# Optimization experiments

Hardware: AMD Instinct MI355X
Metric: run time of the kernel (lower is better)

Reference implementation:

```python
import jax, jax.numpy as jnp
import numpy as np

H, V, B, S = 2048, 32000, 16, 256

def setup_inputs() -> dict:
    key = jax.random.key(0)
    k1, k2, k3, k4 = jax.random.split(key, 4)
    # Parameters exactly as the torch __init__ builds them
    alpha_exp = jax.nn.softmax(jax.random.normal(k1, (H, H), dtype=jnp.float32), axis=1)   # transition probs [H,H]
    beta = jax.nn.log_softmax(jax.random.normal(k2, (H, V), dtype=jnp.float32), axis=1)    # emission log-probs [H,V]
    gamma = jax.nn.log_softmax(jax.random.normal(k3, (H,), dtype=jnp.float32), axis=0)     # initial-state logits [H]
    input_ids = jax.random.randint(k4, (B, S), 0, V)
    return {"input_ids": input_ids, "alpha_exp": alpha_exp, "beta": beta, "gamma": gamma}


def _hmm_forward(input_ids, alpha_exp, beta, gamma):
    # gamma stored as log-probs; forward re-softmaxes it (faithful to torch code)
    gamma_exp = jax.nn.softmax(gamma)                       # [H]
    ids = input_ids.T                                       # [S,B]
    mask = (ids != -1).astype(beta.dtype)                   # [S,B]; -1 = padding
    # input_probs[t,h,b] = beta[h, ids[t,b]] * mask
    ip = jnp.transpose(beta[:, ids], (1, 0, 2)) * mask[:, None, :]   # [S,H,B]
    ip_rev = ip[::-1]                                       # process t = S-1 .. 0

    def step(y, ipt):
        # log-domain backward recursion: y' = log(alpha_exp @ exp(y - ymax)) + ymax + emission
        ymax = jnp.max(y, axis=0, keepdims=True)            # [1,B]
        y = jnp.log(alpha_exp @ jnp.exp(y - ymax)) + ymax + ipt
        return y, y

    y0 = ip_rev[0]                                          # t = S-1: y starts at 0, += emission
    y_last, ys_rest = jax.lax.scan(step, y0, ip_rev[1:])
    ys = jnp.concatenate([y0[None], ys_rest], axis=0)       # [S,H,B], ys[i] is t = S-1-i

    ymax = jnp.max(y_last, axis=0)                          # [B]
    final = jnp.log(gamma_exp @ jnp.exp(y_last - ymax[None, :])) + ymax   # [B] per-seq loglik
    return ys, final


def reference(input_ids, alpha_exp, beta, gamma):
    return _hmm_forward(input_ids, alpha_exp, beta, gamma)
```

## Files before the change

### kernel.cpp

```cpp
#include <hip/hip_runtime.h>
#include <cstdint>
#include <cstddef>

#define Hh 2048
#define Vv 32000
#define Bb 16
#define Ss 256

typedef unsigned short ushort_t;
typedef unsigned int   uint_t;
typedef unsigned long long ull_t;

typedef __attribute__((ext_vector_type(8))) short short8;
typedef __attribute__((ext_vector_type(4))) float f32x4;

#define Z_SLOT   ((size_t)Bb * Hh * 2)
#define WS_NEED  ((size_t)3 * Z_SLOT)

#define LD_REL(p)     __hip_atomic_load((p), __ATOMIC_RELAXED, __HIP_MEMORY_SCOPE_AGENT)
#define ST_REL(p, v)  __hip_atomic_store((p), (v), __ATOMIC_RELAXED, __HIP_MEMORY_SCOPE_AGENT)

#define SGN64 0x8000800080008000ull
#define MAG64 0x7FFF7FFF7FFF7FFFull

__device__ __forceinline__ float b2f_u(uint_t u) {
  union { uint_t u; float f; } x; x.u = u; return x.f;
}
__device__ __forceinline__ ushort_t f2b(float f) {
  union { float f; uint_t u; } x; x.f = f;
  uint_t u = x.u;
  return (ushort_t)((u + 0x7FFFu + ((u >> 16) & 1u)) >> 16);
}
__device__ __forceinline__ uint_t umaxu(uint_t a, uint_t b) { return a > b ? a : b; }
__device__ __forceinline__ uint_t pkmax16(uint_t a, uint_t b) {
  uint_t lo = umaxu(a & 0xFFFFu, b & 0xFFFFu);
  uint_t hi = umaxu(a >> 16, b >> 16);
  return lo | (hi << 16);
}

__global__ __launch_bounds__(256, 1) void hmm_persist(
    const float* __restrict__ alpha,
    const float* __restrict__ beta,
    const int*  __restrict__ ids,
    const float* __restrict__ gamma,
    ushort_t* __restrict__ Zbuf,
    float* __restrict__ out)
{
  const int w    = blockIdx.x;
  const int g    = w & 7;
  const int wl   = w >> 3;
  const int c0   = g * 2;
  const int tid  = threadIdx.x;
  const int wv   = tid >> 6;
  const int lane = tid & 63;
  const int lrow = lane & 15;
  const int quad = lane >> 4;

  __shared__ __align__(16) ushort_t zTf[2 * 2080];
  __shared__ float ybuf[128];
  __shared__ float ipld[128];
  __shared__ uint_t redm[4];
  __shared__ __align__(16) float red[4][4][256];
  __shared__ float fred[4][4];
  __shared__ float mh2[2];

  ull_t* ZbA = (ull_t*)Zbuf;

  short8 afr[64];
  #pragma unroll
  for (int t = 0; t < 4; ++t) {
    #pragma unroll
    for (int kt = 0; kt < 16; ++kt) {
      const float* arow = alpha + (size_t)(wl * 64 + t * 16 + lrow) * Hh
                          + wv * 512 + kt * 32 + quad * 8;
      float4 f0 = *(const float4*)arow;
      float4 f1 = *(const float4*)(arow + 4);
      short8 fr;
      fr[0] = (short)f2b(f0.x); fr[1] = (short)f2b(f0.y);
      fr[2] = (short)f2b(f0.z); fr[3] = (short)f2b(f0.w);
      fr[4] = (short)f2b(f1.x); fr[5] = (short)f2b(f1.y);
      fr[6] = (short)f2b(f1.z); fr[7] = (short)f2b(f1.w);
      afr[t * 16 + kt] = fr;
    }
  }

  const int myc = tid & 1;
  const int myr = wl * 64 + (tid >> 1);
  float ipreg = 0.f;

  {
    if (tid < 128) {
      const int v = ids[(c0 + myc) * Ss + (Ss - 1)];
      float yv = beta[(size_t)myr * Vv + v];
      ybuf[tid] = yv;
      out[(size_t)myr * Bb + (c0 + myc)] = yv;
    }
    __syncthreads();
    if (tid < 32) {
      const int c = tid >> 4, q = tid & 15;
      uint_t b0 = f2b(__expf(ybuf[(q * 4 + 0) * 2 + c]));
      uint_t b1 = f2b(__expf(ybuf[(q * 4 + 1) * 2 + c]));
      uint_t b2 = f2b(__expf(ybuf[(q * 4 + 2) * 2 + c]));
      uint_t b3 = f2b(__expf(ybuf[(q * 4 + 3) * 2 + c]));
      ull_t val = (ull_t)(b0 | (b1 << 16)) | ((ull_t)(b2 | (b3 << 16)) << 32);
      ST_REL(ZbA + (size_t)(c0 + c) * 512 + (wl * 16 + q), val);
    }
    if (tid < 128) {
      const int v1 = ids[(c0 + myc) * Ss + (Ss - 2)];
      ipreg = beta[(size_t)myr * Vv + v1];
    }
  }

  const size_t go0 = (size_t)c0 * 512 + tid;
  const size_t go1 = (size_t)c0 * 512 + 256 + tid;
  const size_t go2 = (size_t)(c0 + 1) * 512 + tid;
  const size_t go3 = (size_t)(c0 + 1) * 512 + 256 + tid;

  float mprev = 0.f;
  const ushort_t* zbase = zTf + (lrow & 1) * 2080 + quad * 8;

  const int  ec  = lrow;
  const int  rb  = wl * 64 + wv * 16 + quad * 4;
  const bool act = (lrow < 2);
  float pendy[4] = {0.f, 0.f, 0.f, 0.f};

  for (int k = 1; k < Ss; ++k) {
    const int   physR = (3 - ((k - 1) % 3)) % 3;
    const ull_t expS  = ((k - 1) & 1) ? SGN64 : 0ull;
    const size_t sb   = (size_t)physR * 8192;

    ull_t z0 = LD_REL(ZbA + sb + go0), z1 = LD_REL(ZbA + sb + go1);
    ull_t z2 = LD_REL(ZbA + sb + go2), z3 = LD_REL(ZbA + sb + go3);
    while ((((z0 ^ expS) | (z1 ^ expS) | (z2 ^ expS) | (z3 ^ expS)) & SGN64) != 0ull) {
      if ((z0 & SGN64) != expS) z0 = LD_REL(ZbA + sb + go0);
      if ((z1 & SGN64) != expS) z1 = LD_REL(ZbA + sb + go1);
      if ((z2 & SGN64) != expS) z2 = LD_REL(ZbA + sb + go2);
      if ((z3 & SGN64) != expS) z3 = LD_REL(ZbA + sb + go3);
    }

    uint_t m0, m1;
    {
      const ull_t u0 = z0 & MAG64, u1 = z1 & MAG64;
      const ull_t u2 = z2 & MAG64, u3 = z3 & MAG64;
      *(ull_t*)(zTf + tid * 4)               = u0;
      *(ull_t*)(zTf + 1024 + tid * 4)        = u1;
      *(ull_t*)(zTf + 2080 + tid * 4)        = u2;
      *(ull_t*)(zTf + 2080 + 1024 + tid * 4) = u3;
      uint_t t0 = pkmax16(pkmax16((uint_t)u0, (uint_t)(u0 >> 32)),
                          pkmax16((uint_t)u1, (uint_t)(u1 >> 32)));
      uint_t t1 = pkmax16(pkmax16((uint_t)u2, (uint_t)(u2 >> 32)),
                          pkmax16((uint_t)u3, (uint_t)(u3 >> 32)));
      m0 = umaxu(t0 & 0xFFFFu, t0 >> 16);
      m1 = umaxu(t1 & 0xFFFFu, t1 >> 16);
    }
    if (tid < 128) ipld[tid] = ipreg;
    uint_t pk = m0 | (m1 << 16);
    #pragma unroll
    for (int d = 1; d < 64; d <<= 1)
      pk = pkmax16(pk, (uint_t)__shfl_xor((int)pk, d));
    if (lane == 0) redm[wv] = pk;
    __syncthreads();

    if (k > 1 && act) {
      #pragma unroll
      for (int i = 0; i < 4; ++i)
        out[(size_t)(k - 1) * (Hh * Bb) + (size_t)(rb + i) * Bb + (c0 + ec)] = pendy[i];
    }

    float ipv[4];
    #pragma unroll
    for (int i = 0; i < 4; ++i)
      ipv[i] = ipld[(wv * 16 + quad * 4 + i) * 2 + (lrow & 1)];
    const uint_t rr = pkmax16(pkmax16(redm[0], redm[1]),
                              pkmax16(redm[2], redm[3]));
    const uint_t mm = (lrow & 1) ? (rr >> 16) : (rr & 0xFFFFu);
    const float lmax = __logf(b2f_u(mm << 16));

    if (k < Ss - 1 && tid < 128) {
      const int v = ids[(c0 + myc) * Ss + (Ss - 2 - k)];
      ipreg = beta[(size_t)myr * Vv + v];
    }

    f32x4 acc0 = {0.f, 0.f, 0.f, 0.f}, acc1 = acc0, acc2 = acc0, acc3 = acc0;
    #pragma unroll
    for (int kt = 0; kt < 16; ++kt) {
      short8 bfr = *(const short8*)(zbase + (wv * 16 + kt) * 32);
      acc0 = __builtin_amdgcn_mfma_f32_16x16x32_bf16(afr[kt],      bfr, acc0, 0, 0, 0);
      acc1 = __builtin_amdgcn_mfma_f32_16x16x32_bf16(afr[16 + kt], bfr, acc1, 0, 0, 0);
      acc2 = __builtin_amdgcn_mfma_f32_16x16x32_bf16(afr[32 + kt], bfr, acc2, 0, 0, 0);
      acc3 = __builtin_amdgcn_mfma_f32_16x16x32_bf16(afr[48 + kt], bfr, acc3, 0, 0, 0);
    }

    if (wv != 0) *(f32x4*)&red[0][wv][lane * 4] = acc0;
    if (wv != 1) *(f32x4*)&red[1][wv][lane * 4] = acc1;
    if (wv != 2) *(f32x4*)&red[2][wv][lane * 4] = acc2;
    if (wv != 3) *(f32x4*)&red[3][wv][lane * 4] = acc3;
    __syncthreads();
    f32x4 sf = acc0;
    if (wv == 1) sf = acc1;
    else if (wv == 2) sf = acc2;
    else if (wv == 3) sf = acc3;
    #pragma unroll
    for (int v = 0; v < 4; ++v)
      if (v != wv) sf += *(const f32x4*)&red[wv][v][lane * 4];

    const float mnew = mprev + lmax;
    if (act) {
      #pragma unroll
      for (int i = 0; i < 4; ++i)
        pendy[i] = __logf(sf[i]) + mprev + ipv[i];
      uint_t o0 = (uint_t)f2b(__expf(pendy[0] - mnew)) |
                  ((uint_t)f2b(__expf(pendy[1] - mnew)) << 16);
      uint_t o1 = (uint_t)f2b(__expf(pendy[2] - mnew)) |
                  ((uint_t)f2b(__expf(pendy[3] - mnew)) << 16);
      const int   physW = (3 - (k % 3)) % 3;
      const ull_t orS   = (k & 1) ? SGN64 : 0ull;
      ST_REL(ZbA + (size_t)physW * 8192 + (size_t)(c0 + ec) * 512 + (rb >> 2),
             ((ull_t)o0 | ((ull_t)o1 << 32)) | orS);
    }
    mprev = mnew;
  }

  if (act) {
    #pragma unroll
    for (int i = 0; i < 4; ++i)
      out[(size_t)(Ss - 1) * (Hh * Bb) + (size_t)(rb + i) * Bb + (c0 + ec)] = pendy[i];
  }

  if (wl == 0) {
    if (tid < 2) mh2[tid] = mprev;
    __syncthreads();
    float4 ga = *(const float4*)(gamma + 4 * tid);
    float4 gb = *(const float4*)(gamma + 1024 + 4 * tid);
    float gmx = fmaxf(fmaxf(fmaxf(ga.x, ga.y), fmaxf(ga.z, ga.w)),
                      fmaxf(fmaxf(gb.x, gb.y), fmaxf(gb.z, gb.w)));
    #pragma unroll
    for (int d = 1; d < 64; d <<= 1) gmx = fmaxf(gmx, __shfl_xor(gmx, d));
    if (lane == 0) fred[wv][0] = gmx;
    __syncthreads();
    const float gm = fmaxf(fmaxf(fred[0][0], fred[1][0]),
                           fmaxf(fred[2][0], fred[3][0]));
    float wgt[8];
    wgt[0] = __expf(ga.x - gm); wgt[1] = __expf(ga.y - gm);
    wgt[2] = __expf(ga.z - gm); wgt[3] = __expf(ga.w - gm);
    wgt[4] = __expf(gb.x - gm); wgt[5] = __expf(gb.y - gm);
    wgt[6] = __expf(gb.z - gm); wgt[7] = __expf(gb.w - gm);
    float s1 = ((wgt[0] + wgt[1]) + (wgt[2] + wgt[3])) +
               ((wgt[4] + wgt[5]) + (wgt[6] + wgt[7]));
    ull_t z0 = LD_REL(ZbA + go0), z1 = LD_REL(ZbA + go1);
    ull_t z2 = LD_REL(ZbA + go2), z3 = LD_REL(ZbA + go3);
    while ((((z0 ^ SGN64) | (z1 ^ SGN64) | (z2 ^ SGN64) | (z3 ^ SGN64)) & SGN64) != 0ull) {
      if ((z0 & SGN64) != SGN64) z0 = LD_REL(ZbA + go0);
      if ((z1 & SGN64) != SGN64) z1 = LD_REL(ZbA + go1);
      if ((z2 & SGN64) != SGN64) z2 = LD_REL(ZbA + go2);
      if ((z3 & SGN64) != SGN64) z3 = LD_REL(ZbA + go3);
    }
    float s2a = 0.f, s2b = 0.f;
    #pragma unroll
    for (int i = 0; i < 4; ++i) {
      s2a += wgt[i]     * b2f_u(((uint_t)(z0 >> (16 * i)) & 0x7FFFu) << 16);
      s2a += wgt[4 + i] * b2f_u(((uint_t)(z1 >> (16 * i)) & 0x7FFFu) << 16);
      s2b += wgt[i]     * b2f_u(((uint_t)(z2 >> (16 * i)) & 0x7FFFu) << 16);
      s2b += wgt[4 + i] * b2f_u(((uint_t)(z3 >> (16 * i)) & 0x7FFFu) << 16);
    }
    #pragma unroll
    for (int d = 1; d < 64; d <<= 1) {
      s1  += __shfl_xor(s1, d);
      s2a += __shfl_xor(s2a, d);
      s2b += __shfl_xor(s2b, d);
    }
    if (lane == 0) { fred[wv][1] = s1; fred[wv][2] = s2a; fred[wv][3] = s2b; }
    __syncthreads();
    if (tid == 0) {
      float S1 = ((fred[0][1] + fred[1][1]) + (fred[2][1] + fred[3][1]));
      float Sa = ((fred[0][2] + fred[1][2]) + (fred[2][2] + fred[3][2]));
      float Sb = ((fred[0][3] + fred[1][3]) + (fred[2][3] + fred[3][3]));
      const float ls1 = __logf(S1);
      out[(size_t)Ss * Hh * Bb + c0]     = __logf(Sa) - ls1 + mh2[0];
      out[(size_t)Ss * Hh * Bb + c0 + 1] = __logf(Sb) - ls1 + mh2[1];
    }
  }
}

extern "C" void kernel_launch(void* const* d_in, const int* in_sizes, int n_in,
                              void* d_out, int out_size, void* d_ws, size_t ws_size,
                              hipStream_t stream) {
  (void)in_sizes; (void)n_in; (void)out_size;
  const int*   ids   = (const int*)d_in[0];
  const float* alpha = (const float*)d_in[1];
  const float* beta  = (const float*)d_in[2];
  const float* gamma = (const float*)d_in[3];
  float* out = (float*)d_out;
  char* ws = (char*)d_ws;

  if (ws_size < WS_NEED) return;

  ushort_t* Zbuf = (ushort_t*)ws;

  hipMemsetAsync(ws, 0x80, 2 * Z_SLOT, stream);
  hipMemsetAsync(ws + 2 * Z_SLOT, 0x00, Z_SLOT, stream);

  {
    const float* a_alpha = alpha;
    const float* a_beta  = beta;
    const int*   a_ids   = ids;
    const float* a_gamma = gamma;
    ushort_t* a_z = Zbuf;  float* a_out = out;
    void* args[] = {(void*)&a_alpha, (void*)&a_beta, (void*)&a_ids,
                    (void*)&a_gamma, (void*)&a_z, (void*)&a_out};
    hipError_t e = hipLaunchCooperativeKernel((const void*)hmm_persist,
                                              dim3(256), dim3(256), args, 0, stream);
    if (e != hipSuccess) {
      hipLaunchKernelGGL(hmm_persist, dim3(256), dim3(256), 0, stream,
                         alpha, beta, ids, gamma, Zbuf, out);
    }
  }
}
```

Measured before the change: 1.761 ms.

## Remove one per-step block barrier via double-buffered LDS and wave-local Z staging

```diff
diff --git a/kernel.cpp b/kernel.cpp
--- a/kernel.cpp
+++ b/kernel.cpp
@@ -58,9 +58,9 @@
 
   __shared__ __align__(16) ushort_t zTf[2 * 2080];
   __shared__ float ybuf[128];
-  __shared__ float ipld[128];
-  __shared__ uint_t redm[4];
-  __shared__ __align__(16) float red[4][4][256];
+  __shared__ float ipld[2][128];
+  __shared__ uint_t redm[2][4];
+  __shared__ __align__(16) float red[2][4][4][256];
   __shared__ float fred[4][4];
   __shared__ float mh2[2];
 
@@ -109,12 +109,15 @@
       const int v1 = ids[(c0 + myc) * Ss + (Ss - 2)];
       ipreg = beta[(size_t)myr * Vv + v1];
     }
-  }
-
-  const size_t go0 = (size_t)c0 * 512 + tid;
-  const size_t go1 = (size_t)c0 * 512 + 256 + tid;
-  const size_t go2 = (size_t)(c0 + 1) * 512 + tid;
-  const size_t go3 = (size_t)(c0 + 1) * 512 + 256 + tid;
+    __syncthreads();
+  }
+
+  const int h4a = wv * 128 + lane;
+  const int h4b = h4a + 64;
+  const size_t go0 = (size_t)c0 * 512 + h4a;
+  const size_t go1 = (size_t)c0 * 512 + h4b;
+  const size_t go2 = (size_t)(c0 + 1) * 512 + h4a;
+  const size_t go3 = (size_t)(c0 + 1) * 512 + h4b;
 
   float mprev = 0.f;
   const ushort_t* zbase = zTf + (lrow & 1) * 2080 + quad * 8;
@@ -125,6 +128,7 @@
   float pendy[4] = {0.f, 0.f, 0.f, 0.f};
 
   for (int k = 1; k < Ss; ++k) {
+    const int   pb    = k & 1;
     const int   physR = (3 - ((k - 1) % 3)) % 3;
     const ull_t expS  = ((k - 1) & 1) ? SGN64 : 0ull;
     const size_t sb   = (size_t)physR * 8192;
@@ -142,10 +146,10 @@
     {
       const ull_t u0 = z0 & MAG64, u1 = z1 & MAG64;
       const ull_t u2 = z2 & MAG64, u3 = z3 & MAG64;
-      *(ull_t*)(zTf + tid * 4)               = u0;
-      *(ull_t*)(zTf + 1024 + tid * 4)        = u1;
-      *(ull_t*)(zTf + 2080 + tid * 4)        = u2;
-      *(ull_t*)(zTf + 2080 + 1024 + tid * 4) = u3;
+      *(ull_t*)(zTf + 4 * h4a)        = u0;
+      *(ull_t*)(zTf + 4 * h4b)        = u1;
+      *(ull_t*)(zTf + 2080 + 4 * h4a) = u2;
+      *(ull_t*)(zTf + 2080 + 4 * h4b) = u3;
       uint_t t0 = pkmax16(pkmax16((uint_t)u0, (uint_t)(u0 >> 32)),
                           pkmax16((uint_t)u1, (uint_t)(u1 >> 32)));
       uint_t t1 = pkmax16(pkmax16((uint_t)u2, (uint_t)(u2 >> 32)),
@@ -153,28 +157,15 @@
       m0 = umaxu(t0 & 0xFFFFu, t0 >> 16);
       m1 = umaxu(t1 & 0xFFFFu, t1 >> 16);
     }
-    if (tid < 128) ipld[tid] = ipreg;
+    if (tid < 128) ipld[pb][tid] = ipreg;
     uint_t pk = m0 | (m1 << 16);
     #pragma unroll
     for (int d = 1; d < 64; d <<= 1)
       pk = pkmax16(pk, (uint_t)__shfl_xor((int)pk, d));
-    if (lane == 0) redm[wv] = pk;
-    __syncthreads();
-
-    if (k > 1 && act) {
-      #pragma unroll
-      for (int i = 0; i < 4; ++i)
-        out[(size_t)(k - 1) * (Hh * Bb) + (size_t)(rb + i) * Bb + (c0 + ec)] = pendy[i];
-    }
-
-    float ipv[4];
-    #pragma unroll
-    for (int i = 0; i < 4; ++i)
-      ipv[i] = ipld[(wv * 16 + quad * 4 + i) * 2 + (lrow & 1)];
-    const uint_t rr = pkmax16(pkmax16(redm[0], redm[1]),
-                              pkmax16(redm[2], redm[3]));
-    const uint_t mm = (lrow & 1) ? (rr >> 16) : (rr & 0xFFFFu);
-    const float lmax = __logf(b2f_u(mm << 16));
+    if (lane == 0) redm[pb][wv] = pk;
+
+    asm volatile("s_waitcnt lgkmcnt(0)" ::: "memory");
+    __builtin_amdgcn_sched_barrier(0);
 
     if (k < Ss - 1 && tid < 128) {
       const int v = ids[(c0 + myc) * Ss + (Ss - 2 - k)];
@@ -191,10 +182,10 @@
       acc3 = __builtin_amdgcn_mfma_f32_16x16x32_bf16(afr[48 + kt], bfr, acc3, 0, 0, 0);
     }
 
-    if (wv != 0) *(f32x4*)&red[0][wv][lane * 4] = acc0;
-    if (wv != 1) *(f32x4*)&red[1][wv][lane * 4] = acc1;
-    if (wv != 2) *(f32x4*)&red[2][wv][lane * 4] = acc2;
-    if (wv != 3) *(f32x4*)&red[3][wv][lane * 4] = acc3;
+    if (wv != 0) *(f32x4*)&red[pb][0][wv][lane * 4] = acc0;
+    if (wv != 1) *(f32x4*)&red[pb][1][wv][lane * 4] = acc1;
+    if (wv != 2) *(f32x4*)&red[pb][2][wv][lane * 4] = acc2;
+    if (wv != 3) *(f32x4*)&red[pb][3][wv][lane * 4] = acc3;
     __syncthreads();
     f32x4 sf = acc0;
     if (wv == 1) sf = acc1;
@@ -202,21 +193,36 @@
     else if (wv == 3) sf = acc3;
     #pragma unroll
     for (int v = 0; v < 4; ++v)
-      if (v != wv) sf += *(const f32x4*)&red[wv][v][lane * 4];
+      if (v != wv) sf += *(const f32x4*)&red[pb][wv][v][lane * 4];
+
+    const uint_t rr = pkmax16(pkmax16(redm[pb][0], redm[pb][1]),
+                              pkmax16(redm[pb][2], redm[pb][3]));
+    const uint_t mm = (lrow & 1) ? (rr >> 16) : (rr & 0xFFFFu);
+    const float lmax = __logf(b2f_u(mm << 16));
+    float ipv[4];
+    #pragma unroll
+    for (int i = 0; i < 4; ++i)
+      ipv[i] = ipld[pb][(wv * 16 + quad * 4 + i) * 2 + (lrow & 1)];
 
     const float mnew = mprev + lmax;
     if (act) {
+      float yv4[4];
       #pragma unroll
       for (int i = 0; i < 4; ++i)
-        pendy[i] = __logf(sf[i]) + mprev + ipv[i];
-      uint_t o0 = (uint_t)f2b(__expf(pendy[0] - mnew)) |
-                  ((uint_t)f2b(__expf(pendy[1] - mnew)) << 16);
-      uint_t o1 = (uint_t)f2b(__expf(pendy[2] - mnew)) |
-                  ((uint_t)f2b(__expf(pendy[3] - mnew)) << 16);
+        yv4[i] = __logf(sf[i]) + mprev + ipv[i];
+      uint_t o0 = (uint_t)f2b(__expf(yv4[0] - mnew)) |
+                  ((uint_t)f2b(__expf(yv4[1] - mnew)) << 16);
+      uint_t o1 = (uint_t)f2b(__expf(yv4[2] - mnew)) |
+                  ((uint_t)f2b(__expf(yv4[3] - mnew)) << 16);
       const int   physW = (3 - (k % 3)) % 3;
       const ull_t orS   = (k & 1) ? SGN64 : 0ull;
       ST_REL(ZbA + (size_t)physW * 8192 + (size_t)(c0 + ec) * 512 + (rb >> 2),
              ((ull_t)o0 | ((ull_t)o1 << 32)) | orS);
+      #pragma unroll
+      for (int i = 0; i < 4; ++i)
+        out[(size_t)(k - 1) * (Hh * Bb) + (size_t)(rb + i) * Bb + (c0 + ec)] = pendy[i];
+      #pragma unroll
+      for (int i = 0; i < 4; ++i) pendy[i] = yv4[i];
     }
     mprev = mnew;
   }
@@ -230,8 +236,8 @@
   if (wl == 0) {
     if (tid < 2) mh2[tid] = mprev;
     __syncthreads();
-    float4 ga = *(const float4*)(gamma + 4 * tid);
-    float4 gb = *(const float4*)(gamma + 1024 + 4 * tid);
+    float4 ga = *(const float4*)(gamma + wv * 512 + 4 * lane);
+    float4 gb = *(const float4*)(gamma + wv * 512 + 256 + 4 * lane);
     float gmx = fmaxf(fmaxf(fmaxf(ga.x, ga.y), fmaxf(ga.z, ga.w)),
                       fmaxf(fmaxf(gb.x, gb.y), fmaxf(gb.z, gb.w)));
     #pragma unroll
@@ -240,13 +246,13 @@
     __syncthreads();
     const float gm = fmaxf(fmaxf(fred[0][0], fred[1][0]),
                            fmaxf(fred[2][0], fred[3][0]));
-    float wgt[8];
-    wgt[0] = __expf(ga.x - gm); wgt[1] = __expf(ga.y - gm);
-    wgt[2] = __expf(ga.z - gm); wgt[3] = __expf(ga.w - gm);
-    wgt[4] = __expf(gb.x - gm); wgt[5] = __expf(gb.y - gm);
-    wgt[6] = __expf(gb.z - gm); wgt[7] = __expf(gb.w - gm);
-    float s1 = ((wgt[0] + wgt[1]) + (wgt[2] + wgt[3])) +
-               ((wgt[4] + wgt[5]) + (wgt[6] + wgt[7]));
+    float wga[4], wgb[4];
+    wga[0] = __expf(ga.x - gm); wga[1] = __expf(ga.y - gm);
+    wga[2] = __expf(ga.z - gm); wga[3] = __expf(ga.w - gm);
+    wgb[0] = __expf(gb.x - gm); wgb[1] = __expf(gb.y - gm);
+    wgb[2] = __expf(gb.z - gm); wgb[3] = __expf(gb.w - gm);
+    float s1 = ((wga[0] + wga[1]) + (wga[2] + wga[3])) +
+               ((wgb[0] + wgb[1]) + (wgb[2] + wgb[3]));
     ull_t z0 = LD_REL(ZbA + go0), z1 = LD_REL(ZbA + go1);
     ull_t z2 = LD_REL(ZbA + go2), z3 = LD_REL(ZbA + go3);
     while ((((z0 ^ SGN64) | (z1 ^ SGN64) | (z2 ^ SGN64) | (z3 ^ SGN64)) & SGN64) != 0ull) {
@@ -258,10 +264,10 @@
     float s2a = 0.f, s2b = 0.f;
     #pragma unroll
     for (int i = 0; i < 4; ++i) {
-      s2a += wgt[i]     * b2f_u(((uint_t)(z0 >> (16 * i)) & 0x7FFFu) << 16);
-      s2a += wgt[4 + i] * b2f_u(((uint_t)(z1 >> (16 * i)) & 0x7FFFu) << 16);
-      s2b += wgt[i]     * b2f_u(((uint_t)(z2 >> (16 * i)) & 0x7FFFu) << 16);
-      s2b += wgt[4 + i] * b2f_u(((uint_t)(z3 >> (16 * i)) & 0x7FFFu) << 16);
+      s2a += wga[i] * b2f_u(((uint_t)(z0 >> (16 * i)) & 0x7FFFu) << 16);
+      s2a += wgb[i] * b2f_u(((uint_t)(z1 >> (16 * i)) & 0x7FFFu) << 16);
+      s2b += wga[i] * b2f_u(((uint_t)(z2 >> (16 * i)) & 0x7FFFu) << 16);
+      s2b += wgb[i] * b2f_u(((uint_t)(z3 >> (16 * i)) & 0x7FFFu) << 16);
     }
     #pragma unroll
     for (int d = 1; d < 64; d <<= 1) {
```

New measurement: 1.726 ms. 2.0% less time.
